# Kernel optimization log

Measured on AMD Instinct MI355X. Metric: run time of the kernel, lower is better.

Reference implementation:

```python
import jax, jax.numpy as jnp
import numpy as np

B, S, D = 1, 8192, 4096
D_OUT = 4096
FP_FEATURES = 256
BITS = 4
MAXQ = float(2 ** BITS - 1)  # 15.0


def setup_inputs() -> dict:
    key = jax.random.key(0)
    kx, kw, kb, ks = jax.random.split(key, 4)
    x = jax.random.normal(kx, (B, S, D), dtype=jnp.float32)
    weight = jax.random.normal(kw, (D_OUT, D), dtype=jnp.float32) * 0.02
    bias = jax.random.normal(kb, (D_OUT,), dtype=jnp.float32) * 0.02
    # act_scales -> sorted indices; top FP_FEATURES stay in fp, rest quantized
    act_scales = jax.random.uniform(ks, (D,), dtype=jnp.float32)
    order = jnp.argsort(act_scales)
    q_idx = order[:-FP_FEATURES].astype(jnp.int64)
    fp_idx = order[-FP_FEATURES:].astype(jnp.int64)
    return {"x": x, "weight": weight, "bias": bias, "q_idx": q_idx, "fp_idx": fp_idx}


def reference(x, weight, bias, q_idx, fp_idx):
    # gather features to be quantized: [B, S, Dq]
    qf = x[:, :, q_idx]
    # per-token asymmetric quant params (find_params)
    xmin = jnp.minimum(qf.min(axis=-1), 0.0)
    xmax = jnp.maximum(qf.max(axis=-1), 0.0)
    both_zero = (xmin == 0.0) & (xmax == 0.0)
    xmin = jnp.where(both_zero, -1.0, xmin)
    xmax = jnp.where(both_zero, 1.0, xmax)
    scale = ((xmax - xmin) / MAXQ)[..., None]   # [B, S, 1]
    zero = jnp.round(-xmin[..., None] / scale)  # [B, S, 1]
    # asymmetric_quantize (fake quant)
    q = jnp.clip(jnp.round(qf / scale) + zero, 0.0, MAXQ)
    qf = scale * (q - zero)
    # scatter quantized + fp features back into a zeros_like buffer
    mixed = jnp.zeros_like(x)
    mixed = mixed.at[:, :, q_idx].set(qf)
    mixed = mixed.at[:, :, fp_idx].set(x[:, :, fp_idx])
    # wrapped Linear
    return mixed @ weight.T + bias
```

## Files before the change

### kernel.cpp

```cpp
#include <hip/hip_runtime.h>


typedef __attribute__((ext_vector_type(8))) short short8;
typedef __attribute__((ext_vector_type(4))) float f32x4;
typedef __attribute__((ext_vector_type(4))) int int4v;

#define S_ROWS 8192
#define D_IN   4096
#define D_OUTC 4096
#define MAXQF  15.0f

__device__ __forceinline__ unsigned short f2bf(float f) {
  unsigned int u = __float_as_uint(f);
  u += 0x7FFFu + ((u >> 16) & 1u);
  return (unsigned short)(u >> 16);
}

__global__ __launch_bounds__(256) void prep_kernel(const float* __restrict__ x,
                                                   const float* __restrict__ W,
                                                   const int* __restrict__ fp_idx,
                                                   signed char* __restrict__ actq,
                                                   signed char* __restrict__ wq,
                                                   short* __restrict__ xfp,
                                                   short* __restrict__ wfp,
                                                   float* __restrict__ as_,
                                                   float* __restrict__ ws_) {
  const int bid = blockIdx.x;
  const int t = threadIdx.x;
  __shared__ float s_r[4];

  if (bid >= S_ROWS) {
    const int row = bid - S_ROWS;
    const float* wr = W + (size_t)row * D_IN;
    float4 v[4];
    float mx = 0.0f;
#pragma unroll
    for (int i = 0; i < 4; ++i) {
      v[i] = ((const float4*)wr)[i * 256 + t];
      mx = fmaxf(mx, fmaxf(fmaxf(fabsf(v[i].x), fabsf(v[i].y)),
                           fmaxf(fabsf(v[i].z), fabsf(v[i].w))));
    }
#pragma unroll
    for (int d = 32; d > 0; d >>= 1) mx = fmaxf(mx, __shfl_xor(mx, d));
    if ((t & 63) == 0) s_r[t >> 6] = mx;
    __syncthreads();
    mx = fmaxf(fmaxf(s_r[0], s_r[1]), fmaxf(s_r[2], s_r[3]));
    const float wsr = (mx > 0.0f) ? (mx / 127.0f) : 1.0f;

    unsigned int* wrow = (unsigned int*)(wq + (size_t)row * D_IN);
#pragma unroll
    for (int i = 0; i < 4; ++i) {
      const float in[4] = { v[i].x, v[i].y, v[i].z, v[i].w };
      unsigned int pk = 0;
#pragma unroll
      for (int j = 0; j < 4; ++j) {
        int q = (int)fminf(fmaxf(rintf(in[j] / wsr), -127.0f), 127.0f);
        pk |= ((unsigned int)(unsigned char)(signed char)q) << (8 * j);
      }
      wrow[i * 256 + t] = pk;
    }
    wfp[(size_t)row * 256 + t] = (short)f2bf(wr[fp_idx[t]]);
    if (t == 0) ws_[row] = wsr;
    return;
  }

  __shared__ unsigned char fl[4096];
  ((int4*)fl)[t] = make_int4(0, 0, 0, 0);
  __syncthreads();
  fl[fp_idx[t]] = 1;
  __syncthreads();

  const int row = bid;
  const float* xr = x + (size_t)row * D_IN;

  float4 v[4];
  unsigned int fw[4];
  float mn = 0.0f, mx = 0.0f;
#pragma unroll
  for (int i = 0; i < 4; ++i) {
    const int idx = i * 256 + t;
    v[i] = ((const float4*)xr)[idx];
    fw[i] = ((const unsigned int*)fl)[idx];
    if (!(fw[i] & 0x000000FFu)) { mn = fminf(mn, v[i].x); mx = fmaxf(mx, v[i].x); }
    if (!(fw[i] & 0x0000FF00u)) { mn = fminf(mn, v[i].y); mx = fmaxf(mx, v[i].y); }
    if (!(fw[i] & 0x00FF0000u)) { mn = fminf(mn, v[i].z); mx = fmaxf(mx, v[i].z); }
    if (!(fw[i] & 0xFF000000u)) { mn = fminf(mn, v[i].w); mx = fmaxf(mx, v[i].w); }
  }
  __shared__ float s_mn[4];
#pragma unroll
  for (int d = 32; d > 0; d >>= 1) {
    mn = fminf(mn, __shfl_xor(mn, d));
    mx = fmaxf(mx, __shfl_xor(mx, d));
  }
  if ((t & 63) == 0) { s_mn[t >> 6] = mn; s_r[t >> 6] = mx; }
  __syncthreads();
  mn = fminf(fminf(s_mn[0], s_mn[1]), fminf(s_mn[2], s_mn[3]));
  mx = fmaxf(fmaxf(s_r[0], s_r[1]), fmaxf(s_r[2], s_r[3]));
  if (mn == 0.0f && mx == 0.0f) { mn = -1.0f; mx = 1.0f; }
  const float scale = (mx - mn) / MAXQF;
  const float zp = rintf(-mn / scale);
  const int zpi = (int)zp;

  unsigned int* arow = (unsigned int*)(actq + (size_t)row * D_IN);
#pragma unroll
  for (int i = 0; i < 4; ++i) {
    const int idx = i * 256 + t;
    const float in[4] = { v[i].x, v[i].y, v[i].z, v[i].w };
    const unsigned int f = fw[i];
    unsigned int pk = 0;
#pragma unroll
    for (int j = 0; j < 4; ++j) {
      int q = (int)fminf(fmaxf(rintf(in[j] / scale) + zp, 0.0f), MAXQF) - zpi;
      if ((f >> (8 * j)) & 0xFFu) q = 0;
      pk |= ((unsigned int)(unsigned char)(signed char)q) << (8 * j);
    }
    arow[idx] = pk;
  }
  xfp[(size_t)row * 256 + t] = (short)f2bf(xr[fp_idx[t]]);
  if (t == 0) as_[row] = scale;
}


__device__ __forceinline__ void gl2lds16(const void* g, const void* l) {
  __builtin_amdgcn_global_load_lds(
      (const __attribute__((address_space(1))) unsigned int*)g,
      (__attribute__((address_space(3))) unsigned int*)l, 16, 0, 0);
}

#define BARRIER()  asm volatile("s_barrier" ::: "memory")
#define LGKM0()    asm volatile("s_waitcnt lgkmcnt(0)" ::: "memory")

__global__ __launch_bounds__(512, 2) void gemm_i8fp_kernel(
    const signed char* __restrict__ A, const signed char* __restrict__ Bw,
    const short* __restrict__ Afp, const short* __restrict__ Bfp,
    const float* __restrict__ as_, const float* __restrict__ ws_,
    const float* __restrict__ bias, float* __restrict__ C) {
  __shared__ __align__(16) signed char lds[131072];
  const int tid = threadIdx.x;
  const int l   = tid & 63;
  const int w   = tid >> 6;
  const int wr  = w >> 2;
  const int wc  = w & 3;
  const int bid = blockIdx.x;
  const int swz = (bid & 7) * 64 + (bid >> 3);
  const int bm  = swz >> 4;
  const int bn  = swz & 15;

  const int c16  = ((l & 7) ^ (l >> 3)) * 16;
  const int rib0 = (w * 2 + 0) * 8 + (l >> 3);
  const int rib1 = (w * 2 + 1) * 8 + (l >> 3);
  const int d0   = (w * 2 + 0) * 1024;
  const int d1   = (w * 2 + 1) * 1024;

  const signed char* bA00 = A  + (size_t)(bm * 256 +   0 + rib0) * D_IN + c16;
  const signed char* bA01 = A  + (size_t)(bm * 256 +   0 + rib1) * D_IN + c16;
  const signed char* bA10 = A  + (size_t)(bm * 256 + 128 + rib0) * D_IN + c16;
  const signed char* bA11 = A  + (size_t)(bm * 256 + 128 + rib1) * D_IN + c16;
  const signed char* bB00 = Bw + (size_t)(bn * 256 +   0 + rib0) * D_IN + c16;
  const signed char* bB01 = Bw + (size_t)(bn * 256 +   0 + rib1) * D_IN + c16;
  const signed char* bB10 = Bw + (size_t)(bn * 256 + 128 + rib0) * D_IN + c16;
  const signed char* bB11 = Bw + (size_t)(bn * 256 + 128 + rib1) * D_IN + c16;

  gl2lds16(bA00, &lds[0 + d0]);           gl2lds16(bA01, &lds[0 + d1]);
  gl2lds16(bA10, &lds[16384 + d0]);       gl2lds16(bA11, &lds[16384 + d1]);
  gl2lds16(bB00, &lds[32768 + d0]);       gl2lds16(bB01, &lds[32768 + d1]);
  gl2lds16(bB10, &lds[49152 + d0]);       gl2lds16(bB11, &lds[49152 + d1]);
  gl2lds16(bA00 + 128, &lds[65536 + d0]); gl2lds16(bA01 + 128, &lds[65536 + d1]);
  gl2lds16(bA10 + 128, &lds[81920 + d0]); gl2lds16(bA11 + 128, &lds[81920 + d1]);
  asm volatile("s_waitcnt vmcnt(4)" ::: "memory");
  BARRIER();

  const signed char* pA00 = bA00 + 256; const signed char* pA01 = bA01 + 256;
  const signed char* pA10 = bA10 + 256; const signed char* pA11 = bA11 + 256;
  const signed char* pB00 = bB00 + 128; const signed char* pB01 = bB01 + 128;
  const signed char* pB10 = bB10 + 128; const signed char* pB11 = bB11 + 128;

  const int ch0  = ((l >> 4) ^ (l & 7)) * 16;
  const int aoff = wr * 16384 + (l & 15) * 128;
  const int boff = 32768 + (wc >> 1) * 16384 + (wc & 1) * 8192 + (l & 15) * 128;

  union AccU {
    int4v ai[8][4];
    f32x4 af[8][4];
  } u;
#pragma unroll
  for (int m = 0; m < 8; ++m)
#pragma unroll
    for (int n = 0; n < 4; ++n) u.ai[m][n] = int4v{0, 0, 0, 0};

  int bo = 0;

  for (int t = 0; t < 32; ++t) {
    const int nxt = bo ^ 65536;
    int4v a0[4][2], a1[4][2], b[2][2];

#pragma unroll
    for (int m = 0; m < 4; ++m) {
      a0[m][0] = *(const int4v*)&lds[bo + aoff + m * 2048 + ch0];
      a0[m][1] = *(const int4v*)&lds[bo + aoff + m * 2048 + (ch0 ^ 64)];
    }
#pragma unroll
    for (int n = 0; n < 2; ++n) {
      b[n][0] = *(const int4v*)&lds[bo + boff + n * 2048 + ch0];
      b[n][1] = *(const int4v*)&lds[bo + boff + n * 2048 + (ch0 ^ 64)];
    }
    if (t < 31) { gl2lds16(pB00, &lds[nxt + 32768 + d0]);
                  gl2lds16(pB01, &lds[nxt + 32768 + d1]); }
    asm volatile("s_waitcnt lgkmcnt(8)" ::: "memory");
    BARRIER();
    LGKM0();
    __builtin_amdgcn_s_setprio(1);
#pragma unroll
    for (int m = 0; m < 4; ++m)
#pragma unroll
      for (int n = 0; n < 2; ++n) {
        u.ai[m][n] = __builtin_amdgcn_mfma_i32_16x16x64_i8(a0[m][0], b[n][0], u.ai[m][n], 0, 0, 0);
        u.ai[m][n] = __builtin_amdgcn_mfma_i32_16x16x64_i8(a0[m][1], b[n][1], u.ai[m][n], 0, 0, 0);
      }
    __builtin_amdgcn_s_setprio(0);
    BARRIER();

#pragma unroll
    for (int m = 0; m < 4; ++m) {
      a1[m][0] = *(const int4v*)&lds[bo + aoff + (m + 4) * 2048 + ch0];
      a1[m][1] = *(const int4v*)&lds[bo + aoff + (m + 4) * 2048 + (ch0 ^ 64)];
    }
    if (t < 31) { gl2lds16(pB10, &lds[nxt + 49152 + d0]);
                  gl2lds16(pB11, &lds[nxt + 49152 + d1]); }
    BARRIER();
    LGKM0();
    __builtin_amdgcn_s_setprio(1);
#pragma unroll
    for (int m = 0; m < 4; ++m)
#pragma unroll
      for (int n = 0; n < 2; ++n) {
        u.ai[m + 4][n] = __builtin_amdgcn_mfma_i32_16x16x64_i8(a1[m][0], b[n][0], u.ai[m + 4][n], 0, 0, 0);
        u.ai[m + 4][n] = __builtin_amdgcn_mfma_i32_16x16x64_i8(a1[m][1], b[n][1], u.ai[m + 4][n], 0, 0, 0);
      }
    __builtin_amdgcn_s_setprio(0);
    BARRIER();

#pragma unroll
    for (int n = 0; n < 2; ++n) {
      b[n][0] = *(const int4v*)&lds[bo + boff + (n + 2) * 2048 + ch0];
      b[n][1] = *(const int4v*)&lds[bo + boff + (n + 2) * 2048 + (ch0 ^ 64)];
    }
    if (t < 30) { gl2lds16(pA00, &lds[bo + 0 + d0]);
                  gl2lds16(pA01, &lds[bo + 0 + d1]); }
    BARRIER();
    LGKM0();
    __builtin_amdgcn_s_setprio(1);
#pragma unroll
    for (int m = 0; m < 4; ++m)
#pragma unroll
      for (int n = 0; n < 2; ++n) {
        u.ai[m + 4][n + 2] = __builtin_amdgcn_mfma_i32_16x16x64_i8(a1[m][0], b[n][0], u.ai[m + 4][n + 2], 0, 0, 0);
        u.ai[m + 4][n + 2] = __builtin_amdgcn_mfma_i32_16x16x64_i8(a1[m][1], b[n][1], u.ai[m + 4][n + 2], 0, 0, 0);
      }
    __builtin_amdgcn_s_setprio(0);
    BARRIER();

    if (t < 30) { gl2lds16(pA10, &lds[bo + 16384 + d0]);
                  gl2lds16(pA11, &lds[bo + 16384 + d1]); }
    BARRIER();
    __builtin_amdgcn_s_setprio(1);
#pragma unroll
    for (int m = 0; m < 4; ++m)
#pragma unroll
      for (int n = 0; n < 2; ++n) {
        u.ai[m][n + 2] = __builtin_amdgcn_mfma_i32_16x16x64_i8(a0[m][0], b[n][0], u.ai[m][n + 2], 0, 0, 0);
        u.ai[m][n + 2] = __builtin_amdgcn_mfma_i32_16x16x64_i8(a0[m][1], b[n][1], u.ai[m][n + 2], 0, 0, 0);
      }
    __builtin_amdgcn_s_setprio(0);
    if (t < 30) { asm volatile("s_waitcnt vmcnt(4)" ::: "memory"); }
    else        { asm volatile("s_waitcnt vmcnt(0)" ::: "memory"); }
    BARRIER();

    pA00 += 128; pA01 += 128; pA10 += 128; pA11 += 128;
    pB00 += 128; pB01 += 128; pB10 += 128; pB11 += 128;
    bo = nxt;
  }

  const int row0 = bm * 256 + wr * 128 + ((l >> 4) << 2);
  const int col0 = bn * 256 + wc * 64 + (l & 15);
#pragma unroll
  for (int m = 0; m < 8; ++m)
#pragma unroll
    for (int n = 0; n < 4; ++n) {
      const float wsv = ws_[col0 + n * 16];
      f32x4 tmp;
#pragma unroll
      for (int r = 0; r < 4; ++r)
        tmp[r] = (float)u.ai[m][n][r] * (as_[row0 + m * 16 + r] * wsv);
      u.af[m][n] = tmp;
    }

  short* sh = (short*)lds;
  const int c16s = ((l & 7) ^ (l >> 3)) * 8;
  const int LDK = 256;
  const short* fA00 = Afp + (size_t)(bm * 256 +   0 + rib0) * LDK + c16s;
  const short* fA01 = Afp + (size_t)(bm * 256 +   0 + rib1) * LDK + c16s;
  const short* fA10 = Afp + (size_t)(bm * 256 + 128 + rib0) * LDK + c16s;
  const short* fA11 = Afp + (size_t)(bm * 256 + 128 + rib1) * LDK + c16s;
  const short* fB00 = Bfp + (size_t)(bn * 256 +   0 + rib0) * LDK + c16s;
  const short* fB01 = Bfp + (size_t)(bn * 256 +   0 + rib1) * LDK + c16s;
  const short* fB10 = Bfp + (size_t)(bn * 256 + 128 + rib0) * LDK + c16s;
  const short* fB11 = Bfp + (size_t)(bn * 256 + 128 + rib1) * LDK + c16s;
  const int ds0 = (w * 2 + 0) * 512;
  const int ds1 = (w * 2 + 1) * 512;

  gl2lds16(fA00, &sh[0 + ds0]);          gl2lds16(fA01, &sh[0 + ds1]);
  gl2lds16(fA10, &sh[8192 + ds0]);       gl2lds16(fA11, &sh[8192 + ds1]);
  gl2lds16(fB00, &sh[16384 + ds0]);      gl2lds16(fB01, &sh[16384 + ds1]);
  gl2lds16(fB10, &sh[24576 + ds0]);      gl2lds16(fB11, &sh[24576 + ds1]);
  gl2lds16(fA00 + 64, &sh[32768 + ds0]); gl2lds16(fA01 + 64, &sh[32768 + ds1]);
  gl2lds16(fA10 + 64, &sh[40960 + ds0]); gl2lds16(fA11 + 64, &sh[40960 + ds1]);
  asm volatile("s_waitcnt vmcnt(4)" ::: "memory");
  BARRIER();

  const short* qA00 = fA00 + 128; const short* qA01 = fA01 + 128;
  const short* qA10 = fA10 + 128; const short* qA11 = fA11 + 128;
  const short* qB00 = fB00 + 64;  const short* qB01 = fB01 + 64;
  const short* qB10 = fB10 + 64;  const short* qB11 = fB11 + 64;

  const int ch0s  = ((l >> 4) ^ (l & 7)) * 8;
  const int aoffs = wr * 8192 + (l & 15) * 64;
  const int boffs = 16384 + (wc >> 1) * 8192 + (wc & 1) * 4096 + (l & 15) * 64;

  int sbo = 0;
  for (int t = 0; t < 4; ++t) {
    const int nxt = sbo ^ 32768;
    short8 a0[4][2], a1[4][2], b[2][2];

#pragma unroll
    for (int m = 0; m < 4; ++m) {
      a0[m][0] = *(const short8*)&sh[sbo + aoffs + m * 1024 + ch0s];
      a0[m][1] = *(const short8*)&sh[sbo + aoffs + m * 1024 + (ch0s ^ 32)];
    }
#pragma unroll
    for (int n = 0; n < 2; ++n) {
      b[n][0] = *(const short8*)&sh[sbo + boffs + n * 1024 + ch0s];
      b[n][1] = *(const short8*)&sh[sbo + boffs + n * 1024 + (ch0s ^ 32)];
    }
    if (t < 3) { gl2lds16(qB00, &sh[nxt + 16384 + ds0]);
                 gl2lds16(qB01, &sh[nxt + 16384 + ds1]); }
    asm volatile("s_waitcnt lgkmcnt(8)" ::: "memory");
    BARRIER();
    LGKM0();
    __builtin_amdgcn_s_setprio(1);
#pragma unroll
    for (int m = 0; m < 4; ++m)
#pragma unroll
      for (int n = 0; n < 2; ++n) {
        u.af[m][n] = __builtin_amdgcn_mfma_f32_16x16x32_bf16(a0[m][0], b[n][0], u.af[m][n], 0, 0, 0);
        u.af[m][n] = __builtin_amdgcn_mfma_f32_16x16x32_bf16(a0[m][1], b[n][1], u.af[m][n], 0, 0, 0);
      }
    __builtin_amdgcn_s_setprio(0);
    BARRIER();

#pragma unroll
    for (int m = 0; m < 4; ++m) {
      a1[m][0] = *(const short8*)&sh[sbo + aoffs + (m + 4) * 1024 + ch0s];
      a1[m][1] = *(const short8*)&sh[sbo + aoffs + (m + 4) * 1024 + (ch0s ^ 32)];
    }
    if (t < 3) { gl2lds16(qB10, &sh[nxt + 24576 + ds0]);
                 gl2lds16(qB11, &sh[nxt + 24576 + ds1]); }
    BARRIER();
    LGKM0();
    __builtin_amdgcn_s_setprio(1);
#pragma unroll
    for (int m = 0; m < 4; ++m)
#pragma unroll
      for (int n = 0; n < 2; ++n) {
        u.af[m + 4][n] = __builtin_amdgcn_mfma_f32_16x16x32_bf16(a1[m][0], b[n][0], u.af[m + 4][n], 0, 0, 0);
        u.af[m + 4][n] = __builtin_amdgcn_mfma_f32_16x16x32_bf16(a1[m][1], b[n][1], u.af[m + 4][n], 0, 0, 0);
      }
    __builtin_amdgcn_s_setprio(0);
    BARRIER();

#pragma unroll
    for (int n = 0; n < 2; ++n) {
      b[n][0] = *(const short8*)&sh[sbo + boffs + (n + 2) * 1024 + ch0s];
      b[n][1] = *(const short8*)&sh[sbo + boffs + (n + 2) * 1024 + (ch0s ^ 32)];
    }
    if (t < 2) { gl2lds16(qA00, &sh[sbo + 0 + ds0]);
                 gl2lds16(qA01, &sh[sbo + 0 + ds1]); }
    BARRIER();
    LGKM0();
    __builtin_amdgcn_s_setprio(1);
#pragma unroll
    for (int m = 0; m < 4; ++m)
#pragma unroll
      for (int n = 0; n < 2; ++n) {
        u.af[m + 4][n + 2] = __builtin_amdgcn_mfma_f32_16x16x32_bf16(a1[m][0], b[n][0], u.af[m + 4][n + 2], 0, 0, 0);
        u.af[m + 4][n + 2] = __builtin_amdgcn_mfma_f32_16x16x32_bf16(a1[m][1], b[n][1], u.af[m + 4][n + 2], 0, 0, 0);
      }
    __builtin_amdgcn_s_setprio(0);
    BARRIER();

    if (t < 2) { gl2lds16(qA10, &sh[sbo + 8192 + ds0]);
                 gl2lds16(qA11, &sh[sbo + 8192 + ds1]); }
    BARRIER();
    __builtin_amdgcn_s_setprio(1);
#pragma unroll
    for (int m = 0; m < 4; ++m)
#pragma unroll
      for (int n = 0; n < 2; ++n) {
        u.af[m][n + 2] = __builtin_amdgcn_mfma_f32_16x16x32_bf16(a0[m][0], b[n][0], u.af[m][n + 2], 0, 0, 0);
        u.af[m][n + 2] = __builtin_amdgcn_mfma_f32_16x16x32_bf16(a0[m][1], b[n][1], u.af[m][n + 2], 0, 0, 0);
      }
    __builtin_amdgcn_s_setprio(0);
    if (t < 2) { asm volatile("s_waitcnt vmcnt(4)" ::: "memory"); }
    else       { asm volatile("s_waitcnt vmcnt(0)" ::: "memory"); }
    BARRIER();

    qA00 += 64; qA01 += 64; qA10 += 64; qA11 += 64;
    qB00 += 64; qB01 += 64; qB10 += 64; qB11 += 64;
    sbo = nxt;
  }

#pragma unroll
  for (int m = 0; m < 8; ++m)
#pragma unroll
    for (int n = 0; n < 4; ++n) {
      const int col = col0 + n * 16;
      const float bv = bias[col];
#pragma unroll
      for (int r = 0; r < 4; ++r)
        C[(size_t)(row0 + m * 16 + r) * D_OUTC + col] = u.af[m][n][r] + bv;
    }
}

extern "C" void kernel_launch(void* const* d_in, const int* in_sizes, int n_in,
                              void* d_out, int out_size, void* d_ws, size_t ws_size,
                              hipStream_t stream) {
  const float* x    = (const float*)d_in[0];
  const float* W    = (const float*)d_in[1];
  const float* bias = (const float*)d_in[2];
  const int* fp_idx = (const int*)d_in[4];

  char* ws = (char*)d_ws;
  signed char* actq = (signed char*)ws;
  signed char* wq   = (signed char*)(ws + (32u << 20));
  short* xfp        = (short*)(ws + (48u << 20));
  short* wfp        = (short*)(ws + (52u << 20));
  float* as_        = (float*)(ws + (54u << 20));
  float* ws_        = (float*)(ws + (54u << 20) + (64u << 10));
  float* out = (float*)d_out;

  prep_kernel<<<S_ROWS + D_OUTC, 256, 0, stream>>>(x, W, fp_idx, actq, wq,
                                                   xfp, wfp, as_, ws_);
  gemm_i8fp_kernel<<<512, 512, 0, stream>>>(actq, wq, xfp, wfp, as_, ws_,
                                            bias, out);
}
```

Baseline: 231.4 us.

## Replace double-buffered fp-feature GEMM tail with simple single-buffer load-compute loop

The fp-feature (K=256) tail of the GEMM drops its double-buffered, interleaved prefetch schedule with priority hints. Each K-step now loads the A and B tiles into one LDS buffer, waits for all loads, then runs every MFMA for the step. This removes the complex barrier and pipelining machinery and cuts register pressure from holding split A/B fragments. In exchange, global loads no longer overlap with compute in this short tail.

```diff
diff --git a/kernel.cpp b/kernel.cpp
--- a/kernel.cpp
+++ b/kernel.cpp
@@ -297,126 +297,46 @@
 
   short* sh = (short*)lds;
   const int c16s = ((l & 7) ^ (l >> 3)) * 8;
-  const int LDK = 256;
-  const short* fA00 = Afp + (size_t)(bm * 256 +   0 + rib0) * LDK + c16s;
-  const short* fA01 = Afp + (size_t)(bm * 256 +   0 + rib1) * LDK + c16s;
-  const short* fA10 = Afp + (size_t)(bm * 256 + 128 + rib0) * LDK + c16s;
-  const short* fA11 = Afp + (size_t)(bm * 256 + 128 + rib1) * LDK + c16s;
-  const short* fB00 = Bfp + (size_t)(bn * 256 +   0 + rib0) * LDK + c16s;
-  const short* fB01 = Bfp + (size_t)(bn * 256 +   0 + rib1) * LDK + c16s;
-  const short* fB10 = Bfp + (size_t)(bn * 256 + 128 + rib0) * LDK + c16s;
-  const short* fB11 = Bfp + (size_t)(bn * 256 + 128 + rib1) * LDK + c16s;
+  const short* fA = Afp + (size_t)(bm * 256 + rib0) * 256 + c16s;
+  const short* fB = Bfp + (size_t)(bn * 256 + rib0) * 256 + c16s;
   const int ds0 = (w * 2 + 0) * 512;
   const int ds1 = (w * 2 + 1) * 512;
-
-  gl2lds16(fA00, &sh[0 + ds0]);          gl2lds16(fA01, &sh[0 + ds1]);
-  gl2lds16(fA10, &sh[8192 + ds0]);       gl2lds16(fA11, &sh[8192 + ds1]);
-  gl2lds16(fB00, &sh[16384 + ds0]);      gl2lds16(fB01, &sh[16384 + ds1]);
-  gl2lds16(fB10, &sh[24576 + ds0]);      gl2lds16(fB11, &sh[24576 + ds1]);
-  gl2lds16(fA00 + 64, &sh[32768 + ds0]); gl2lds16(fA01 + 64, &sh[32768 + ds1]);
-  gl2lds16(fA10 + 64, &sh[40960 + ds0]); gl2lds16(fA11 + 64, &sh[40960 + ds1]);
-  asm volatile("s_waitcnt vmcnt(4)" ::: "memory");
-  BARRIER();
-
-  const short* qA00 = fA00 + 128; const short* qA01 = fA01 + 128;
-  const short* qA10 = fA10 + 128; const short* qA11 = fA11 + 128;
-  const short* qB00 = fB00 + 64;  const short* qB01 = fB01 + 64;
-  const short* qB10 = fB10 + 64;  const short* qB11 = fB11 + 64;
 
   const int ch0s  = ((l >> 4) ^ (l & 7)) * 8;
   const int aoffs = wr * 8192 + (l & 15) * 64;
   const int boffs = 16384 + (wc >> 1) * 8192 + (wc & 1) * 4096 + (l & 15) * 64;
 
-  int sbo = 0;
   for (int t = 0; t < 4; ++t) {
-    const int nxt = sbo ^ 32768;
-    short8 a0[4][2], a1[4][2], b[2][2];
-
-#pragma unroll
-    for (int m = 0; m < 4; ++m) {
-      a0[m][0] = *(const short8*)&sh[sbo + aoffs + m * 1024 + ch0s];
-      a0[m][1] = *(const short8*)&sh[sbo + aoffs + m * 1024 + (ch0s ^ 32)];
-    }
-#pragma unroll
-    for (int n = 0; n < 2; ++n) {
-      b[n][0] = *(const short8*)&sh[sbo + boffs + n * 1024 + ch0s];
-      b[n][1] = *(const short8*)&sh[sbo + boffs + n * 1024 + (ch0s ^ 32)];
-    }
-    if (t < 3) { gl2lds16(qB00, &sh[nxt + 16384 + ds0]);
-                 gl2lds16(qB01, &sh[nxt + 16384 + ds1]); }
-    asm volatile("s_waitcnt lgkmcnt(8)" ::: "memory");
-    BARRIER();
+    const int ko = t * 64;
+    gl2lds16(fA + ko,         &sh[0 + ds0]);
+    gl2lds16(fA + 2048 + ko,  &sh[0 + ds1]);
+    gl2lds16(fA + 32768 + ko, &sh[8192 + ds0]);
+    gl2lds16(fA + 34816 + ko, &sh[8192 + ds1]);
+    gl2lds16(fB + ko,         &sh[16384 + ds0]);
+    gl2lds16(fB + 2048 + ko,  &sh[16384 + ds1]);
+    gl2lds16(fB + 32768 + ko, &sh[24576 + ds0]);
+    gl2lds16(fB + 34816 + ko, &sh[24576 + ds1]);
+    asm volatile("s_waitcnt vmcnt(0)" ::: "memory");
+    BARRIER();
+
+    short8 bf[4][2];
+#pragma unroll
+    for (int n = 0; n < 4; ++n) {
+      bf[n][0] = *(const short8*)&sh[boffs + n * 1024 + ch0s];
+      bf[n][1] = *(const short8*)&sh[boffs + n * 1024 + (ch0s ^ 32)];
+    }
+#pragma unroll
+    for (int mi = 0; mi < 8; ++mi) {
+      short8 av0 = *(const short8*)&sh[aoffs + mi * 1024 + ch0s];
+      short8 av1 = *(const short8*)&sh[aoffs + mi * 1024 + (ch0s ^ 32)];
+#pragma unroll
+      for (int n = 0; n < 4; ++n) {
+        u.af[mi][n] = __builtin_amdgcn_mfma_f32_16x16x32_bf16(av0, bf[n][0], u.af[mi][n], 0, 0, 0);
+        u.af[mi][n] = __builtin_amdgcn_mfma_f32_16x16x32_bf16(av1, bf[n][1], u.af[mi][n], 0, 0, 0);
+      }
+    }
     LGKM0();
-    __builtin_amdgcn_s_setprio(1);
-#pragma unroll
-    for (int m = 0; m < 4; ++m)
-#pragma unroll
-      for (int n = 0; n < 2; ++n) {
-        u.af[m][n] = __builtin_amdgcn_mfma_f32_16x16x32_bf16(a0[m][0], b[n][0], u.af[m][n], 0, 0, 0);
-        u.af[m][n] = __builtin_amdgcn_mfma_f32_16x16x32_bf16(a0[m][1], b[n][1], u.af[m][n], 0, 0, 0);
-      }
-    __builtin_amdgcn_s_setprio(0);
-    BARRIER();
-
-#pragma unroll
-    for (int m = 0; m < 4; ++m) {
-      a1[m][0] = *(const short8*)&sh[sbo + aoffs + (m + 4) * 1024 + ch0s];
-      a1[m][1] = *(const short8*)&sh[sbo + aoffs + (m + 4) * 1024 + (ch0s ^ 32)];
-    }
-    if (t < 3) { gl2lds16(qB10, &sh[nxt + 24576 + ds0]);
-                 gl2lds16(qB11, &sh[nxt + 24576 + ds1]); }
-    BARRIER();
-    LGKM0();
-    __builtin_amdgcn_s_setprio(1);
-#pragma unroll
-    for (int m = 0; m < 4; ++m)
-#pragma unroll
-      for (int n = 0; n < 2; ++n) {
-        u.af[m + 4][n] = __builtin_amdgcn_mfma_f32_16x16x32_bf16(a1[m][0], b[n][0], u.af[m + 4][n], 0, 0, 0);
-        u.af[m + 4][n] = __builtin_amdgcn_mfma_f32_16x16x32_bf16(a1[m][1], b[n][1], u.af[m + 4][n], 0, 0, 0);
-      }
-    __builtin_amdgcn_s_setprio(0);
-    BARRIER();
-
-#pragma unroll
-    for (int n = 0; n < 2; ++n) {
-      b[n][0] = *(const short8*)&sh[sbo + boffs + (n + 2) * 1024 + ch0s];
-      b[n][1] = *(const short8*)&sh[sbo + boffs + (n + 2) * 1024 + (ch0s ^ 32)];
-    }
-    if (t < 2) { gl2lds16(qA00, &sh[sbo + 0 + ds0]);
-                 gl2lds16(qA01, &sh[sbo + 0 + ds1]); }
-    BARRIER();
-    LGKM0();
-    __builtin_amdgcn_s_setprio(1);
-#pragma unroll
-    for (int m = 0; m < 4; ++m)
-#pragma unroll
-      for (int n = 0; n < 2; ++n) {
-        u.af[m + 4][n + 2] = __builtin_amdgcn_mfma_f32_16x16x32_bf16(a1[m][0], b[n][0], u.af[m + 4][n + 2], 0, 0, 0);
-        u.af[m + 4][n + 2] = __builtin_amdgcn_mfma_f32_16x16x32_bf16(a1[m][1], b[n][1], u.af[m + 4][n + 2], 0, 0, 0);
-      }
-    __builtin_amdgcn_s_setprio(0);
-    BARRIER();
-
-    if (t < 2) { gl2lds16(qA10, &sh[sbo + 8192 + ds0]);
-                 gl2lds16(qA11, &sh[sbo + 8192 + ds1]); }
-    BARRIER();
-    __builtin_amdgcn_s_setprio(1);
-#pragma unroll
-    for (int m = 0; m < 4; ++m)
-#pragma unroll
-      for (int n = 0; n < 2; ++n) {
-        u.af[m][n + 2] = __builtin_amdgcn_mfma_f32_16x16x32_bf16(a0[m][0], b[n][0], u.af[m][n + 2], 0, 0, 0);
-        u.af[m][n + 2] = __builtin_amdgcn_mfma_f32_16x16x32_bf16(a0[m][1], b[n][1], u.af[m][n + 2], 0, 0, 0);
-      }
-    __builtin_amdgcn_s_setprio(0);
-    if (t < 2) { asm volatile("s_waitcnt vmcnt(4)" ::: "memory"); }
-    else       { asm volatile("s_waitcnt vmcnt(0)" ::: "memory"); }
-    BARRIER();
-
-    qA00 += 64; qA01 += 64; qA10 += 64; qA11 += 64;
-    qB00 += 64; qB01 += 64; qB10 += 64; qB11 += 64;
-    sbo = nxt;
+    BARRIER();
   }
 
 #pragma unroll
```

New measurement: 207.5 us (median of 2 runs). 10.3% less time.
